# Kernel optimization log

Measured on AMD Instinct MI355X. Metric: run time of the kernel, lower is better.

The kernel has to match this reference:

```python
import jax, jax.numpy as jnp
import numpy as np

N_NODES = 50000
N_EDGES = 1600000
F_IN = 512      # 2 * embedding_dimension
HID = 512
OUT = 4
NEG_SLOPE = 0.01  # torch LeakyReLU default


def _leaky_relu(x):
    return jnp.where(x >= 0, x, NEG_SLOPE * x)


def setup_inputs() -> dict:
    key = jax.random.key(0)
    ks = jax.random.split(key, 12)
    s_in = 1.0 / np.sqrt(F_IN)
    s_h = 1.0 / np.sqrt(HID)
    return {
        "feature": jax.random.normal(ks[0], (N_NODES, F_IN), jnp.float32),
        "edge_index": jax.random.randint(ks[1], (2, N_EDGES), 0, N_NODES, jnp.int64),
        "edge_type": jax.random.randint(ks[2], (N_EDGES,), 0, 2, jnp.int64),
        # input MLP
        "W_in": jax.random.uniform(ks[3], (F_IN, HID), jnp.float32, -s_in, s_in),
        "b_in": jnp.zeros((HID,), jnp.float32),
        # sage1: lin_l (bias) on aggregated neighbors, lin_r (no bias) on self
        "W1_l": jax.random.uniform(ks[4], (HID, HID), jnp.float32, -s_h, s_h),
        "b1_l": jnp.zeros((HID,), jnp.float32),
        "W1_r": jax.random.uniform(ks[5], (HID, HID), jnp.float32, -s_h, s_h),
        # sage2
        "W2_l": jax.random.uniform(ks[6], (HID, HID), jnp.float32, -s_h, s_h),
        "b2_l": jnp.zeros((HID,), jnp.float32),
        "W2_r": jax.random.uniform(ks[7], (HID, HID), jnp.float32, -s_h, s_h),
        # output linear (hidden -> 4); note forward skips linear_relu_output1
        "W_out": jax.random.uniform(ks[8], (HID, OUT), jnp.float32, -s_h, s_h),
        "b_out": jnp.zeros((OUT,), jnp.float32),
    }


def _sage_conv(x, src, dst, W_l, b_l, W_r):
    # mean aggregation of source features onto destinations (PyG default flow)
    agg = jax.ops.segment_sum(x[src], dst, num_segments=N_NODES)  # [N, H]
    cnt = jax.ops.segment_sum(jnp.ones((src.shape[0], 1), x.dtype), dst,
                              num_segments=N_NODES)               # [N, 1]
    mean = agg / jnp.maximum(cnt, 1.0)
    return mean @ W_l + b_l + x @ W_r


def reference(feature, edge_index, edge_type,
              W_in, b_in, W1_l, b1_l, W1_r, W2_l, b2_l, W2_r, W_out, b_out):
    src, dst = edge_index[0], edge_index[1]
    x = _leaky_relu(feature.astype(jnp.float32) @ W_in + b_in)
    x = _sage_conv(x, src, dst, W1_l, b1_l, W1_r)
    # dropout is identity in eval mode
    x = _sage_conv(x, src, dst, W2_l, b2_l, W2_r)
    return x @ W_out + b_out
```

## Files before the change

### kernel.cpp

```cpp
#include <hip/hip_runtime.h>
#include <stdint.h>

#define NNODES 50000
#define NEDGES 1600000
#define HID 512
#define NEG_SLOPE 0.01f
#define NBUCK 98
#define NBLK 200
#define TILE 8000
#define NSUB 8
#define GPBLK 391

typedef __attribute__((ext_vector_type(8))) short bf16x8;
typedef __attribute__((ext_vector_type(8))) unsigned short u16x8;
typedef __attribute__((ext_vector_type(4))) float f32x4;

__device__ __forceinline__ float bf2f(unsigned short u) {
  unsigned int x = ((unsigned int)u) << 16;
  return __builtin_bit_cast(float, x);
}
__device__ __forceinline__ unsigned short f2bf(float f) {
  unsigned int u = __builtin_bit_cast(unsigned int, f);
  u += 0x7FFFu + ((u >> 16) & 1u);
  return (unsigned short)(u >> 16);
}

__global__ void flagk(const int* __restrict__ ei, int* __restrict__ flag) {
  int t = threadIdx.x;
  unsigned long long m = __ballot(ei[2 * t + 1] != 0);
  if (t == 0) *flag = (m != 0ULL) ? 1 : 0;
}

__global__ __launch_bounds__(256) void histk(const int* __restrict__ ei,
                                             const int* __restrict__ flag,
                                             int* __restrict__ hist) {
  __shared__ int h[NBUCK];
  int t = threadIdx.x, blk = blockIdx.x;
  for (int i = t; i < NBUCK; i += 256) h[i] = 0;
  __syncthreads();
  int f = *flag;
  int e0 = blk * TILE;
  for (int e = e0 + 2 * t; e < e0 + TILE; e += 512) {
    int d0, d1;
    if (f) {
      int2 v = *reinterpret_cast<const int2*>(&ei[(size_t)NEDGES + e]);
      d0 = v.x; d1 = v.y;
    } else {
      int4 v = *reinterpret_cast<const int4*>(&ei[2 * ((size_t)NEDGES + e)]);
      d0 = v.x; d1 = v.z;
    }
    if ((unsigned)d0 < NNODES) atomicAdd(&h[d0 >> 9], 1);
    if ((unsigned)d1 < NNODES) atomicAdd(&h[d1 >> 9], 1);
  }
  __syncthreads();
  for (int i = t; i < NBUCK; i += 256) hist[i * NBLK + blk] = h[i];
}

__global__ __launch_bounds__(512) void scanh(int* __restrict__ hist,
                                             int* __restrict__ bstart) {
  __shared__ int s[512];
  const int TOT = NBUCK * NBLK;
  const int C = 40;
  int t = threadIdx.x;
  int base = t * C;
  int sum = 0;
#pragma unroll
  for (int i = 0; i < C; i++) {
    int idx = base + i;
    sum += (idx < TOT) ? hist[idx] : 0;
  }
  s[t] = sum;
  __syncthreads();
  for (int off = 1; off < 512; off <<= 1) {
    int u = (t >= off) ? s[t - off] : 0;
    __syncthreads();
    s[t] += u;
    __syncthreads();
  }
  int run = (t > 0) ? s[t - 1] : 0;
#pragma unroll
  for (int i = 0; i < C; i++) {
    int idx = base + i;
    if (idx < TOT) {
      int v = hist[idx];
      hist[idx] = run;
      if (idx % NBLK == 0) bstart[idx / NBLK] = run;
      run += v;
    }
  }
  if (t == 511) bstart[NBUCK] = s[511];
}

__global__ __launch_bounds__(256) void binscatter(const int* __restrict__ ei,
                                                  const int* __restrict__ flag,
                                                  const int* __restrict__ hbase,
                                                  unsigned int* __restrict__ pcol) {
  __shared__ int lb[NBUCK];
  int t = threadIdx.x, blk = blockIdx.x;
  for (int i = t; i < NBUCK; i += 256) lb[i] = hbase[i * NBLK + blk];
  __syncthreads();
  int f = *flag;
  int e0 = blk * TILE;
  for (int e = e0 + 2 * t; e < e0 + TILE; e += 512) {
    int s0, s1, d0, d1;
    if (f) {
      int2 vs = *reinterpret_cast<const int2*>(&ei[e]);
      int2 vd = *reinterpret_cast<const int2*>(&ei[(size_t)NEDGES + e]);
      s0 = vs.x; s1 = vs.y; d0 = vd.x; d1 = vd.y;
    } else {
      int4 vs = *reinterpret_cast<const int4*>(&ei[2 * (size_t)e]);
      int4 vd = *reinterpret_cast<const int4*>(&ei[2 * ((size_t)NEDGES + e)]);
      s0 = vs.x; s1 = vs.z; d0 = vd.x; d1 = vd.z;
    }
    if ((unsigned)d0 < NNODES) {
      if ((unsigned)s0 >= NNODES) s0 = 0;
      int pos = atomicAdd(&lb[d0 >> 9], 1);
      pcol[pos] = ((unsigned)(d0 & 511) << 16) | (unsigned)s0;
    }
    if ((unsigned)d1 < NNODES) {
      if ((unsigned)s1 >= NNODES) s1 = 0;
      int pos = atomicAdd(&lb[d1 >> 9], 1);
      pcol[pos] = ((unsigned)(d1 & 511) << 16) | (unsigned)s1;
    }
  }
}

__global__ void tcast(const float* __restrict__ w, unsigned short* __restrict__ wt) {
  int i = blockIdx.x * 256 + threadIdx.x;
  int n = i >> 9, k = i & 511;
  wt[i] = f2bf(w[(k << 9) | n]);
}

__device__ __forceinline__ float wave_dot(const float* __restrict__ Arow,
                                          const float* __restrict__ B, int j) {
  int l = threadIdx.x & 63;
  float4 a0 = *reinterpret_cast<const float4*>(Arow + l * 8);
  float4 a1 = *reinterpret_cast<const float4*>(Arow + l * 8 + 4);
  const float* bb = B + (size_t)(l * 8) * 4 + j;
  float s = a0.x * bb[0] + a0.y * bb[4] + a0.z * bb[8] + a0.w * bb[12] +
            a1.x * bb[16] + a1.y * bb[20] + a1.z * bb[24] + a1.w * bb[28];
#pragma unroll
  for (int off = 1; off < 64; off <<= 1) s += __shfl_xor(s, off);
  return s;
}

__global__ __launch_bounds__(256) void smallA(
    const float* __restrict__ W2l, const float* __restrict__ W2r,
    const float* __restrict__ Wout, const float* __restrict__ b2l,
    const float* __restrict__ bout,
    float* __restrict__ Wlp, float* __restrict__ Wrp, float* __restrict__ bp) {
  int gw = blockIdx.x * 4 + (threadIdx.x >> 6);
  int l = threadIdx.x & 63;
  if (gw < 2048) {
    float v = wave_dot(W2l + (size_t)(gw >> 2) * 512, Wout, gw & 3);
    if (l == 0) Wlp[gw] = v;
  } else if (gw < 4096) {
    int g = gw - 2048;
    float v = wave_dot(W2r + (size_t)(g >> 2) * 512, Wout, g & 3);
    if (l == 0) Wrp[g] = v;
  } else if (gw < 4100) {
    int j = gw - 4096;
    float v = wave_dot(b2l, Wout, j);
    if (l == 0) bp[j] = v + bout[j];
  }
}

__global__ __launch_bounds__(256) void smallB(
    const float* __restrict__ W1l, const float* __restrict__ W1r,
    const float* __restrict__ b1l,
    const float* __restrict__ Wlp, const float* __restrict__ Wrp,
    const float* __restrict__ bp,
    float* __restrict__ Pall, float* __restrict__ kb, float* __restrict__ kc) {
  int gw = blockIdx.x * 4 + (threadIdx.x >> 6);
  int l = threadIdx.x & 63;
  if (gw < 6144) {
    int k = gw / 12, jg = gw % 12;
    int g = jg >> 2, j = jg & 3;
    float v;
    if (g == 0) v = wave_dot(W1l + (size_t)k * 512, Wlp, j);
    else if (g == 1) v = wave_dot(W1r + (size_t)k * 512, Wlp, j) +
                         wave_dot(W1l + (size_t)k * 512, Wrp, j);
    else v = wave_dot(W1r + (size_t)k * 512, Wrp, j);
    if (l == 0) Pall[k * 12 + jg] = v;
  } else if (gw < 6152) {
    int i = gw - 6144, j = i & 3;
    if (i < 4) {
      float v = wave_dot(b1l, Wlp, j);
      if (l == 0) kb[j] = v;
    } else {
      float v = wave_dot(b1l, Wrp, j);
      if (l == 0) kc[j] = v + bp[j];
    }
  }
}

__global__ __launch_bounds__(512) void gemmproj(
    const float* __restrict__ A, const unsigned short* __restrict__ Bt,
    const float* __restrict__ bias, const float* __restrict__ Pall,
    float* __restrict__ t0) {
  __shared__ __align__(16) char smem[51200];
  unsigned short* As = (unsigned short*)smem;
  unsigned short* Bs = (unsigned short*)(smem + 10240);
  __shared__ float tab[128 * 12];
  const int tid = threadIdx.x;
  const int wv = tid >> 6, lane = tid & 63;
  const int bm = blockIdx.x * 128;
  const int wr = wv >> 2, wc = wv & 3;
  const int r15 = lane & 15, kl = lane >> 4;

  for (int i = tid; i < 1536; i += 512) tab[i] = 0.f;

  f32x4 acc[8][4];
#pragma unroll
  for (int ni = 0; ni < 8; ni++)
#pragma unroll
    for (int mi = 0; mi < 4; mi++) acc[ni][mi] = {0.f, 0.f, 0.f, 0.f};

  const int arow = tid >> 2;
  const int ak8 = (tid & 3) * 8;
  int garow = bm + arow;
  if (garow >= NNODES) garow = 0;
  const float* gabase = A + (size_t)garow * HID + ak8;

  for (int kt = 0; kt < 16; ++kt) {
    const float* ga = gabase + kt * 32;
    float4 v0 = *reinterpret_cast<const float4*>(ga);
    float4 v1 = *reinterpret_cast<const float4*>(ga + 4);
    u16x8 pk;
    pk[0] = f2bf(v0.x); pk[1] = f2bf(v0.y); pk[2] = f2bf(v0.z); pk[3] = f2bf(v0.w);
    pk[4] = f2bf(v1.x); pk[5] = f2bf(v1.y); pk[6] = f2bf(v1.z); pk[7] = f2bf(v1.w);
    *reinterpret_cast<u16x8*>(&As[arow * 40 + ak8]) = pk;
#pragma unroll
    for (int i = 0; i < 4; ++i) {
      int c = i * 512 + tid;
      int n = c >> 2, slot = c & 3;
      uint4 bv = *reinterpret_cast<const uint4*>(Bt + (size_t)n * HID + kt * 32 + slot * 8);
      *reinterpret_cast<uint4*>(&Bs[n * 40 + slot * 8]) = bv;
    }
    __syncthreads();
    bf16x8 af[4], bfr[8];
#pragma unroll
    for (int mi = 0; mi < 4; ++mi)
      af[mi] = *reinterpret_cast<const bf16x8*>(&As[(wr * 64 + mi * 16 + r15) * 40 + kl * 8]);
#pragma unroll
    for (int ni = 0; ni < 8; ++ni)
      bfr[ni] = *reinterpret_cast<const bf16x8*>(&Bs[(wc * 128 + ni * 16 + r15) * 40 + kl * 8]);
#pragma unroll
    for (int ni = 0; ni < 8; ++ni)
#pragma unroll
      for (int mi = 0; mi < 4; ++mi)
        acc[ni][mi] = __builtin_amdgcn_mfma_f32_16x16x32_bf16(bfr[ni], af[mi], acc[ni][mi], 0, 0, 0);
    __syncthreads();
  }

  float part[4][12];
#pragma unroll
  for (int mi = 0; mi < 4; ++mi)
#pragma unroll
    for (int j = 0; j < 12; ++j) part[mi][j] = 0.f;

#pragma unroll
  for (int ni = 0; ni < 8; ++ni) {
    int nb = wc * 128 + ni * 16 + kl * 4;
    float4 bv4 = *reinterpret_cast<const float4*>(bias + nb);
    float bb[4] = {bv4.x, bv4.y, bv4.z, bv4.w};
#pragma unroll
    for (int rg = 0; rg < 4; ++rg) {
      const float* Pc = Pall + (size_t)(nb + rg) * 12;
      float4 p0 = *reinterpret_cast<const float4*>(Pc);
      float4 p1 = *reinterpret_cast<const float4*>(Pc + 4);
      float4 p2 = *reinterpret_cast<const float4*>(Pc + 8);
#pragma unroll
      for (int mi = 0; mi < 4; ++mi) {
        float v = acc[ni][mi][rg] + bb[rg];
        v = (v >= 0.f) ? v : NEG_SLOPE * v;
        part[mi][0] += v * p0.x; part[mi][1] += v * p0.y;
        part[mi][2] += v * p0.z; part[mi][3] += v * p0.w;
        part[mi][4] += v * p1.x; part[mi][5] += v * p1.y;
        part[mi][6] += v * p1.z; part[mi][7] += v * p1.w;
        part[mi][8] += v * p2.x; part[mi][9] += v * p2.y;
        part[mi][10] += v * p2.z; part[mi][11] += v * p2.w;
      }
    }
  }
#pragma unroll
  for (int mi = 0; mi < 4; ++mi)
#pragma unroll
    for (int j = 0; j < 12; ++j) {
      part[mi][j] += __shfl_xor(part[mi][j], 16);
      part[mi][j] += __shfl_xor(part[mi][j], 32);
    }
  if (kl == 0) {
#pragma unroll
    for (int mi = 0; mi < 4; ++mi) {
      int r = wr * 64 + mi * 16 + r15;
#pragma unroll
      for (int j = 0; j < 12; ++j) atomicAdd(&tab[r * 12 + j], part[mi][j]);
    }
  }
  __syncthreads();
  for (int i = tid; i < 1536; i += 512) {
    int r = i / 12;
    int gr = bm + r;
    if (gr < NNODES) t0[(size_t)gr * 12 + (i - r * 12)] = tab[i];
  }
}

__global__ __launch_bounds__(256) void aggA(
    const unsigned int* __restrict__ pcol, const int* __restrict__ bstart,
    const float* __restrict__ t0, float* __restrict__ partial) {
  __shared__ float tab[512 * 5];
  int t = threadIdx.x;
  int b = blockIdx.x >> 3, sb = blockIdx.x & 7;
  for (int i = t; i < 2560; i += 256) tab[i] = 0.f;
  __syncthreads();
  int st = bstart[b], en = bstart[b + 1];
  int len = en - st;
  int a0 = st + (int)(((long long)len * sb) >> 3);
  int a1 = st + (int)(((long long)len * (sb + 1)) >> 3);
  for (int e = a0 + t; e < a1; e += 256) {
    unsigned v = pcol[e];
    int i = v >> 16, src = v & 0xFFFF;
    float4 x = *reinterpret_cast<const float4*>(t0 + (size_t)src * 12);
    atomicAdd(&tab[i * 5 + 0], x.x);
    atomicAdd(&tab[i * 5 + 1], x.y);
    atomicAdd(&tab[i * 5 + 2], x.z);
    atomicAdd(&tab[i * 5 + 3], x.w);
    atomicAdd(&tab[i * 5 + 4], 1.f);
  }
  __syncthreads();
  float* o = partial + (size_t)blockIdx.x * 2560;
  for (int i = t; i < 2560; i += 256) o[i] = tab[i];
}

__global__ __launch_bounds__(256) void finA(
    const float* __restrict__ partial, const float* __restrict__ t0,
    float* __restrict__ s1, float* __restrict__ degf) {
  int n = blockIdx.x * 256 + threadIdx.x;
  if (n >= NNODES) return;
  int b = n >> 9, i = n & 511;
  float a[5] = {0.f, 0.f, 0.f, 0.f, 0.f};
#pragma unroll
  for (int s = 0; s < 8; s++) {
    const float* p = partial + (size_t)(b * 8 + s) * 2560 + i * 5;
#pragma unroll
    for (int j = 0; j < 5; j++) a[j] += p[j];
  }
  float deg = a[4];
  float sc = (deg > 0.f) ? 1.f / deg : 0.f;
  float4 tb = *reinterpret_cast<const float4*>(t0 + (size_t)n * 12 + 4);
  float4 o = {a[0] * sc + tb.x, a[1] * sc + tb.y, a[2] * sc + tb.z, a[3] * sc + tb.w};
  *reinterpret_cast<float4*>(s1 + (size_t)n * 4) = o;
  degf[n] = deg;
}

__global__ __launch_bounds__(256) void aggB(
    const unsigned int* __restrict__ pcol, const int* __restrict__ bstart,
    const float* __restrict__ s1, float* __restrict__ partial) {
  __shared__ float tab[512 * 4];
  int t = threadIdx.x;
  int b = blockIdx.x >> 3, sb = blockIdx.x & 7;
  for (int i = t; i < 2048; i += 256) tab[i] = 0.f;
  __syncthreads();
  int st = bstart[b], en = bstart[b + 1];
  int len = en - st;
  int a0 = st + (int)(((long long)len * sb) >> 3);
  int a1 = st + (int)(((long long)len * (sb + 1)) >> 3);
  for (int e = a0 + t; e < a1; e += 256) {
    unsigned v = pcol[e];
    int i = v >> 16, src = v & 0xFFFF;
    float4 x = *reinterpret_cast<const float4*>(s1 + (size_t)src * 4);
    atomicAdd(&tab[i * 4 + 0], x.x);
    atomicAdd(&tab[i * 4 + 1], x.y);
    atomicAdd(&tab[i * 4 + 2], x.z);
    atomicAdd(&tab[i * 4 + 3], x.w);
  }
  __syncthreads();
  float* o = partial + (size_t)blockIdx.x * 2048;
  for (int i = t; i < 2048; i += 256) o[i] = tab[i];
}

__global__ __launch_bounds__(256) void finB(
    const float* __restrict__ partial, const float* __restrict__ t0,
    const float* __restrict__ degf, const float* __restrict__ kb,
    const float* __restrict__ kc, float* __restrict__ out) {
  int n = blockIdx.x * 256 + threadIdx.x;
  if (n >= NNODES) return;
  int b = n >> 9, i = n & 511;
  float a[4] = {0.f, 0.f, 0.f, 0.f};
#pragma unroll
  for (int s = 0; s < 8; s++) {
    const float* p = partial + (size_t)(b * 8 + s) * 2048 + i * 4;
#pragma unroll
    for (int j = 0; j < 4; j++) a[j] += p[j];
  }
  float deg = degf[n];
  float sc = (deg > 0.f) ? 1.f / deg : 0.f;
  float ind = (deg > 0.f) ? 1.f : 0.f;
  float4 c = *reinterpret_cast<const float4*>(t0 + (size_t)n * 12 + 8);
  float4 vb = *reinterpret_cast<const float4*>(kb);
  float4 vc = *reinterpret_cast<const float4*>(kc);
  float4 o = {a[0] * sc + c.x + ind * vb.x + vc.x,
              a[1] * sc + c.y + ind * vb.y + vc.y,
              a[2] * sc + c.z + ind * vb.z + vc.z,
              a[3] * sc + c.w + ind * vb.w + vc.w};
  *reinterpret_cast<float4*>(out + (size_t)n * 4) = o;
}

extern "C" void kernel_launch(void* const* d_in, const int* in_sizes, int n_in,
                              void* d_out, int out_size, void* d_ws, size_t ws_size,
                              hipStream_t stream) {
  const float* feat = (const float*)d_in[0];
  const int* ei = (const int*)d_in[1];
  const float* W_in = (const float*)d_in[3];
  const float* b_in = (const float*)d_in[4];
  const float* W1l = (const float*)d_in[5];
  const float* b1l = (const float*)d_in[6];
  const float* W1r = (const float*)d_in[7];
  const float* W2l = (const float*)d_in[8];
  const float* b2l = (const float*)d_in[9];
  const float* W2r = (const float*)d_in[10];
  const float* Wout = (const float*)d_in[11];
  const float* bout = (const float*)d_in[12];
  float* out = (float*)d_out;

  char* ws = (char*)d_ws;
  size_t off = 0;
  auto alloc = [&](size_t bytes) {
    void* p = ws + off;
    off += (bytes + 15) & ~(size_t)15;
    return p;
  };
  int* flag   = (int*)alloc(16);
  int* hist   = (int*)alloc((size_t)NBUCK * NBLK * 4);
  int* bstart = (int*)alloc((NBUCK + 1) * 4);
  unsigned int* pcol = (unsigned int*)alloc((size_t)NEDGES * 4);
  unsigned short* Wt0 = (unsigned short*)alloc(512 * 512 * 2);
  float* Wlp  = (float*)alloc(2048 * 4);
  float* Wrp  = (float*)alloc(2048 * 4);
  float* bp   = (float*)alloc(16);
  float* Pall = (float*)alloc(512 * 12 * 4);
  float* kb   = (float*)alloc(16);
  float* kc   = (float*)alloc(16);
  float* t0   = (float*)alloc((size_t)NNODES * 12 * 4);
  float* s1   = (float*)alloc((size_t)NNODES * 4 * 4);
  float* degf = (float*)alloc((size_t)NNODES * 4);
  float* partial = (float*)alloc((size_t)NBUCK * NSUB * 2560 * 4);
  (void)ws_size;

  flagk<<<1, 64, 0, stream>>>(ei, flag);
  histk<<<NBLK, 256, 0, stream>>>(ei, flag, hist);
  scanh<<<1, 512, 0, stream>>>(hist, bstart);
  binscatter<<<NBLK, 256, 0, stream>>>(ei, flag, hist, pcol);

  tcast<<<1024, 256, 0, stream>>>(W_in, Wt0);
  smallA<<<1025, 256, 0, stream>>>(W2l, W2r, Wout, b2l, bout, Wlp, Wrp, bp);
  smallB<<<1538, 256, 0, stream>>>(W1l, W1r, b1l, Wlp, Wrp, bp, Pall, kb, kc);

  gemmproj<<<GPBLK, 512, 0, stream>>>(feat, Wt0, b_in, Pall, t0);
  aggA<<<NBUCK * NSUB, 256, 0, stream>>>(pcol, bstart, t0, partial);
  finA<<<(NNODES + 255) / 256, 256, 0, stream>>>(partial, t0, s1, degf);
  aggB<<<NBUCK * NSUB, 256, 0, stream>>>(pcol, bstart, s1, partial);
  finB<<<(NNODES + 255) / 256, 256, 0, stream>>>(partial, t0, degf, kb, kc, out);
}
```

Before: 284.5 us.

## Split input GEMM over four N-tiles with grouped scheduling and partial reduction

The fused input GEMM plus projection kernel used to give each 512-thread block a full 128x512 output slab. It now launches 128x128 tiles with 256 threads, ordered so that groups of 8 M-tiles share an N-tile, and loads B into LDS directly with global_load_lds. Each N-tile writes its 12-column projected partials to a separate buffer, and a new small kernel sums the four partials. The point is to get more blocks and better occupancy than the 391 large blocks gave. The cost is reading the fp32 A rows four times with four bf16 conversions, one extra launch, and an extra partial buffer.

```diff
diff --git a/kernel.cpp b/kernel.cpp
--- a/kernel.cpp
+++ b/kernel.cpp
@@ -10,6 +10,7 @@
 #define TILE 8000
 #define NSUB 8
 #define GPBLK 391
+#define MROWS 50048
 
 typedef __attribute__((ext_vector_type(8))) short bf16x8;
 typedef __attribute__((ext_vector_type(8))) unsigned short u16x8;
@@ -23,6 +24,11 @@
   unsigned int u = __builtin_bit_cast(unsigned int, f);
   u += 0x7FFFu + ((u >> 16) & 1u);
   return (unsigned short)(u >> 16);
+}
+__device__ __forceinline__ void gload_lds16(const void* g, void* l) {
+  __builtin_amdgcn_global_load_lds(
+      (const __attribute__((address_space(1))) void*)g,
+      (__attribute__((address_space(3))) void*)l, 16, 0, 0);
 }
 
 __global__ void flagk(const int* __restrict__ ei, int* __restrict__ flag) {
@@ -194,59 +200,63 @@
   }
 }
 
-__global__ __launch_bounds__(512) void gemmproj(
+__global__ __launch_bounds__(256) void gemmproj(
     const float* __restrict__ A, const unsigned short* __restrict__ Bt,
     const float* __restrict__ bias, const float* __restrict__ Pall,
-    float* __restrict__ t0) {
-  __shared__ __align__(16) char smem[51200];
-  unsigned short* As = (unsigned short*)smem;
-  unsigned short* Bs = (unsigned short*)(smem + 10240);
+    float* __restrict__ t0p) {
+  __shared__ unsigned short As[128 * 32];
+  __shared__ unsigned short Bs[128 * 32];
   __shared__ float tab[128 * 12];
   const int tid = threadIdx.x;
-  const int wv = tid >> 6, lane = tid & 63;
-  const int bm = blockIdx.x * 128;
-  const int wr = wv >> 2, wc = wv & 3;
+  const int wave = tid >> 6, lane = tid & 63;
+  const int w = blockIdx.x;
+  const int mt = (w & 7) + ((w >> 5) << 3);
+  const int nb = (w >> 3) & 3;
+  if (mt >= GPBLK) return;
+  const int bm = mt * 128, bn = nb * 128;
+  const int wr = wave >> 1, wc = wave & 1;
   const int r15 = lane & 15, kl = lane >> 4;
-
-  for (int i = tid; i < 1536; i += 512) tab[i] = 0.f;
-
-  f32x4 acc[8][4];
-#pragma unroll
-  for (int ni = 0; ni < 8; ni++)
-#pragma unroll
-    for (int mi = 0; mi < 4; mi++) acc[ni][mi] = {0.f, 0.f, 0.f, 0.f};
-
-  const int arow = tid >> 2;
-  const int ak8 = (tid & 3) * 8;
-  int garow = bm + arow;
-  if (garow >= NNODES) garow = 0;
-  const float* gabase = A + (size_t)garow * HID + ak8;
-
-  for (int kt = 0; kt < 16; ++kt) {
-    const float* ga = gabase + kt * 32;
-    float4 v0 = *reinterpret_cast<const float4*>(ga);
-    float4 v1 = *reinterpret_cast<const float4*>(ga + 4);
-    u16x8 pk;
-    pk[0] = f2bf(v0.x); pk[1] = f2bf(v0.y); pk[2] = f2bf(v0.z); pk[3] = f2bf(v0.w);
-    pk[4] = f2bf(v1.x); pk[5] = f2bf(v1.y); pk[6] = f2bf(v1.z); pk[7] = f2bf(v1.w);
-    *reinterpret_cast<u16x8*>(&As[arow * 40 + ak8]) = pk;
-#pragma unroll
-    for (int i = 0; i < 4; ++i) {
-      int c = i * 512 + tid;
-      int n = c >> 2, slot = c & 3;
-      uint4 bv = *reinterpret_cast<const uint4*>(Bt + (size_t)n * HID + kt * 32 + slot * 8);
-      *reinterpret_cast<uint4*>(&Bs[n * 40 + slot * 8]) = bv;
+  const int srow = lane >> 2, soff = (lane & 3) * 8;
+
+  for (int i = tid; i < 1536; i += 256) tab[i] = 0.f;
+
+  f32x4 acc[4][4];
+#pragma unroll
+  for (int i = 0; i < 4; i++)
+#pragma unroll
+    for (int j = 0; j < 4; j++) acc[i][j] = {0.f, 0.f, 0.f, 0.f};
+
+  for (int kt = 0; kt < HID / 32; ++kt) {
+#pragma unroll
+    for (int rr = 0; rr < 2; ++rr) {
+      int c = wave * 2 + rr;
+      int row = c * 16 + srow;
+      gload_lds16(Bt + (size_t)(bn + row) * HID + kt * 32 + soff, (void*)&Bs[c * 512]);
+    }
+#pragma unroll
+    for (int ss = 0; ss < 2; ++ss) {
+      int s = tid + ss * 256;
+      int row = s >> 2, k8 = (s & 3) * 8;
+      int garow = bm + row;
+      if (garow >= NNODES) garow = 0;
+      const float* ga = A + (size_t)garow * HID + kt * 32 + k8;
+      float4 v0 = *reinterpret_cast<const float4*>(ga);
+      float4 v1 = *reinterpret_cast<const float4*>(ga + 4);
+      u16x8 pk;
+      pk[0] = f2bf(v0.x); pk[1] = f2bf(v0.y); pk[2] = f2bf(v0.z); pk[3] = f2bf(v0.w);
+      pk[4] = f2bf(v1.x); pk[5] = f2bf(v1.y); pk[6] = f2bf(v1.z); pk[7] = f2bf(v1.w);
+      *reinterpret_cast<u16x8*>(&As[row * 32 + k8]) = pk;
     }
     __syncthreads();
-    bf16x8 af[4], bfr[8];
+    bf16x8 af[4], bfr[4];
 #pragma unroll
     for (int mi = 0; mi < 4; ++mi)
-      af[mi] = *reinterpret_cast<const bf16x8*>(&As[(wr * 64 + mi * 16 + r15) * 40 + kl * 8]);
-#pragma unroll
-    for (int ni = 0; ni < 8; ++ni)
-      bfr[ni] = *reinterpret_cast<const bf16x8*>(&Bs[(wc * 128 + ni * 16 + r15) * 40 + kl * 8]);
-#pragma unroll
-    for (int ni = 0; ni < 8; ++ni)
+      af[mi] = *reinterpret_cast<const bf16x8*>(&As[(wr * 64 + mi * 16 + r15) * 32 + kl * 8]);
+#pragma unroll
+    for (int ni = 0; ni < 4; ++ni)
+      bfr[ni] = *reinterpret_cast<const bf16x8*>(&Bs[(wc * 64 + ni * 16 + r15) * 32 + kl * 8]);
+#pragma unroll
+    for (int ni = 0; ni < 4; ++ni)
 #pragma unroll
       for (int mi = 0; mi < 4; ++mi)
         acc[ni][mi] = __builtin_amdgcn_mfma_f32_16x16x32_bf16(bfr[ni], af[mi], acc[ni][mi], 0, 0, 0);
@@ -260,13 +270,13 @@
     for (int j = 0; j < 12; ++j) part[mi][j] = 0.f;
 
 #pragma unroll
-  for (int ni = 0; ni < 8; ++ni) {
-    int nb = wc * 128 + ni * 16 + kl * 4;
-    float4 bv4 = *reinterpret_cast<const float4*>(bias + nb);
+  for (int ni = 0; ni < 4; ++ni) {
+    int nbase = bn + wc * 64 + ni * 16 + kl * 4;
+    float4 bv4 = *reinterpret_cast<const float4*>(bias + nbase);
     float bb[4] = {bv4.x, bv4.y, bv4.z, bv4.w};
 #pragma unroll
     for (int rg = 0; rg < 4; ++rg) {
-      const float* Pc = Pall + (size_t)(nb + rg) * 12;
+      const float* Pc = Pall + (size_t)(nbase + rg) * 12;
       float4 p0 = *reinterpret_cast<const float4*>(Pc);
       float4 p1 = *reinterpret_cast<const float4*>(Pc + 4);
       float4 p2 = *reinterpret_cast<const float4*>(Pc + 8);
@@ -299,11 +309,16 @@
     }
   }
   __syncthreads();
-  for (int i = tid; i < 1536; i += 512) {
-    int r = i / 12;
-    int gr = bm + r;
-    if (gr < NNODES) t0[(size_t)gr * 12 + (i - r * 12)] = tab[i];
-  }
+  float* o = t0p + (size_t)nb * MROWS * 12 + (size_t)bm * 12;
+  for (int i = tid; i < 1536; i += 256) o[i] = tab[i];
+}
+
+__global__ __launch_bounds__(256) void reduce_t0(const float* __restrict__ t0p,
+                                                 float* __restrict__ t0) {
+  int i = blockIdx.x * 256 + threadIdx.x;
+  if (i >= NNODES * 12) return;
+  const size_t S = (size_t)MROWS * 12;
+  t0[i] = t0p[i] + t0p[S + i] + t0p[2 * S + i] + t0p[3 * S + i];
 }
 
 __global__ __launch_bounds__(256) void aggA(
@@ -443,6 +458,7 @@
   float* kb   = (float*)alloc(16);
   float* kc   = (float*)alloc(16);
   float* t0   = (float*)alloc((size_t)NNODES * 12 * 4);
+  float* t0p  = (float*)alloc((size_t)4 * MROWS * 12 * 4);
   float* s1   = (float*)alloc((size_t)NNODES * 4 * 4);
   float* degf = (float*)alloc((size_t)NNODES * 4);
   float* partial = (float*)alloc((size_t)NBUCK * NSUB * 2560 * 4);
@@ -457,7 +473,8 @@
   smallA<<<1025, 256, 0, stream>>>(W2l, W2r, Wout, b2l, bout, Wlp, Wrp, bp);
   smallB<<<1538, 256, 0, stream>>>(W1l, W1r, b1l, Wlp, Wrp, bp, Pall, kb, kc);
 
-  gemmproj<<<GPBLK, 512, 0, stream>>>(feat, Wt0, b_in, Pall, t0);
+  gemmproj<<<1568, 256, 0, stream>>>(feat, Wt0, b_in, Pall, t0p);
+  reduce_t0<<<(NNODES * 12 + 255) / 256, 256, 0, stream>>>(t0p, t0);
   aggA<<<NBUCK * NSUB, 256, 0, stream>>>(pcol, bstart, t0, partial);
   finA<<<(NNODES + 255) / 256, 256, 0, stream>>>(partial, t0, s1, degf);
   aggB<<<NBUCK * NSUB, 256, 0, stream>>>(pcol, bstart, s1, partial);
```

Measured after the change: 306.2 us. 7.7% more time.
